# Performance work log

Measured on AMD Instinct MI355X. Metric: run time of the kernel, lower is better.

Reference implementation:

```python
import jax, jax.numpy as jnp
import numpy as np
from jax import lax

B_, DIM, H, W, Dd = 2, 256, 16, 16, 16
DI, N, DTR, K = 256, 8, 16, 4   # d_inner (expand=1), d_state, dt_rank=ceil(256/16), d_conv
OUT_C = 1200
L = H * W * Dd
EPS = 1e-5


def setup_inputs() -> dict:
    key = jax.random.key(0)
    ks = jax.random.split(key, 20)
    g = lambda k, s: jax.random.normal(k, s, jnp.float32) * 0.02
    A_log = jnp.log(jnp.broadcast_to(jnp.arange(1, N + 1, dtype=jnp.float32), (DI, N)))
    dt_bias = jnp.full((DI,), float(np.log(np.expm1(0.01))), jnp.float32)
    return {
        "input0": jax.random.normal(ks[0], (B_, DIM, H, W, Dd), jnp.float32),
        "input1": jax.random.normal(ks[1], (B_, DIM, H, W, Dd), jnp.float32),
        "norm0_w": jnp.ones((DIM,), jnp.float32),
        "norm0_b": jnp.zeros((DIM,), jnp.float32),
        "norm1_w": jnp.ones((DIM,), jnp.float32),
        "norm1_b": jnp.zeros((DIM,), jnp.float32),
        "in_proj_w": g(ks[2], (DI, DIM)),
        "in_projz_w": g(ks[3], (DI, DIM)),
        "conv1d_w": g(ks[4], (DI, 1, K)),
        "conv1d_bias": jnp.zeros((DI,), jnp.float32),
        "conv1db_w": g(ks[5], (DI, 1, K)),
        "conv1db_bias": jnp.zeros((DI,), jnp.float32),
        "xproj_w": g(ks[6], (DTR + 2 * N, DI)),
        "xprojb_w": g(ks[7], (DTR + 2 * N, DI)),
        "dtproj_w": g(ks[8], (DI, DTR)),
        "dtproj_bias": dt_bias,
        "dtprojb_w": g(ks[9], (DI, DTR)),
        "dtprojb_bias": dt_bias,
        "A_log": A_log,
        "Ab_log": A_log,
        "D_p": jnp.ones((DI,), jnp.float32),
        "D_b": jnp.ones((DI,), jnp.float32),
        "rms_w": jnp.ones((DI,), jnp.float32),
        "out_proj_w": g(ks[10], (DIM, DI)),
        "conv3d_w": g(ks[11], (OUT_C, DIM)),
        "conv3d_bias": jnp.zeros((OUT_C,), jnp.float32),
    }


def _layernorm(x, w, b):
    m = x.mean(-1, keepdims=True)
    v = ((x - m) ** 2).mean(-1, keepdims=True)
    return (x - m) * lax.rsqrt(v + EPS) * w + b


def _rmsnorm(x, w):
    return x * lax.rsqrt((x * x).mean(-1, keepdims=True) + EPS) * w


def _ssm_dir(x, z, conv_w, conv_b, xproj_w, dtproj_w, dtproj_bias, A_log, Dp):
    # One direction of the bimamba-v2 selective scan. x, z: (b, L, d_inner)
    xt = x.transpose(0, 2, 1)  # (b, d, L)
    xc = lax.conv_general_dilated(xt, conv_w, (1,), [(K - 1, 0)], feature_group_count=DI)
    x = jax.nn.silu(xc + conv_b[None, :, None]).transpose(0, 2, 1)  # causal dw-conv + silu
    dbl = x @ xproj_w.T                                   # (b, L, dt_rank + 2n)
    dt, Bm, Cm = dbl[..., :DTR], dbl[..., DTR:DTR + N], dbl[..., DTR + N:]
    dt = jax.nn.softplus(dt @ dtproj_w.T + dtproj_bias)    # (b, L, d)
    A = -jnp.exp(A_log)                                    # (d, n)
    dA = jnp.exp(dt[..., None] * A)                        # (b, L, d, n)
    dBu = (dt * x)[..., None] * Bm[:, :, None, :]          # (b, L, d, n)

    def step(h, inp):
        dA_t, dBu_t, C_t = inp
        h = h * dA_t + dBu_t
        return h, jnp.einsum('bdn,bn->bd', h, C_t)

    h0 = jnp.zeros((x.shape[0], DI, N), x.dtype)
    _, ys = lax.scan(step, h0, (dA.transpose(1, 0, 2, 3), dBu.transpose(1, 0, 2, 3), Cm.transpose(1, 0, 2)))
    y = ys.transpose(1, 0, 2) + x * Dp                     # (b, L, d)
    return y * jax.nn.silu(z)                              # gate from the matching branch


def _forward(input0, input1, norm0_w, norm0_b, norm1_w, norm1_b, in_proj_w, in_projz_w,
             conv1d_w, conv1d_bias, conv1db_w, conv1db_bias, xproj_w, xprojb_w,
             dtproj_w, dtproj_bias, dtprojb_w, dtprojb_bias, A_log, Ab_log,
             D_p, D_b, rms_w, out_proj_w, conv3d_w, conv3d_bias):
    b = input0.shape[0]
    skip = input0
    seq0 = input0.transpose(0, 2, 3, 4, 1).reshape(b, L, DIM)  # b (h w d) c
    seq1 = input1.transpose(0, 2, 3, 4, 1).reshape(b, L, DIM)
    seq0 = _layernorm(seq0, norm0_w, norm0_b)
    seq1 = _layernorm(seq1, norm1_w, norm1_b)
    x = seq0 @ in_proj_w.T    # SSM input from input0
    z = seq1 @ in_projz_w.T   # gate from extra_emb (input1)
    y_f = _ssm_dir(x, z, conv1d_w, conv1d_bias, xproj_w, dtproj_w, dtproj_bias, A_log, D_p)
    y_b = _ssm_dir(x[:, ::-1], z[:, ::-1], conv1db_w, conv1db_bias, xprojb_w,
                   dtprojb_w, dtprojb_bias, Ab_log, D_b)[:, ::-1]

    def head(y):
        o = _rmsnorm(y, rms_w) @ out_proj_w.T              # use_norm=True, then out_proj
        o = o.reshape(b, H, W, Dd, DIM).transpose(0, 4, 1, 2, 3) + skip
        return jnp.einsum('bchwd,oc->bohwd', o, conv3d_w) + conv3d_bias[None, :, None, None, None]

    out = head((y_f + y_b) * 0.5)   # if_devide_out=True
    return out, head(y_f), head(y_b)


def reference(input0, input1, norm0_w, norm0_b, norm1_w, norm1_b, in_proj_w, in_projz_w,
              conv1d_w, conv1d_bias, conv1db_w, conv1db_bias, xproj_w, xprojb_w,
              dtproj_w, dtproj_bias, dtprojb_w, dtprojb_bias, A_log, Ab_log,
              D_p, D_b, rms_w, out_proj_w, conv3d_w, conv3d_bias):
    return _forward(input0, input1, norm0_w, norm0_b, norm1_w, norm1_b, in_proj_w, in_projz_w,
                    conv1d_w, conv1d_bias, conv1db_w, conv1db_bias, xproj_w, xprojb_w,
                    dtproj_w, dtproj_bias, dtprojb_w, dtprojb_bias, A_log, Ab_log,
                    D_p, D_b, rms_w, out_proj_w, conv3d_w, conv3d_bias)
```

## Files before the change

kernel.cpp:

```cpp
#include <hip/hip_runtime.h>
#include <cstdint>

#define NTOK 8192

typedef __attribute__((ext_vector_type(4))) float f32x4;
typedef __attribute__((ext_vector_type(8))) short s16x8;
typedef __attribute__((ext_vector_type(4))) short s16x4;

__device__ __forceinline__ short f2bf(float f) {
  union { float f; unsigned u; } x; x.f = f;
  unsigned r = x.u + 0x7FFFu + ((x.u >> 16) & 1u);
  return (short)(r >> 16);
}
__device__ __forceinline__ float bf2f(short s) {
  union { float f; unsigned u; } x;
  x.u = ((unsigned)(unsigned short)s) << 16;
  return x.f;
}
__device__ __forceinline__ void gl_lds16(const void* g, void* l) {
  __builtin_amdgcn_global_load_lds((const unsigned int*)g, (unsigned int*)l, 16, 0, 0);
}

__global__ __launch_bounds__(256) void ln_transpose_kernel(
    const float* __restrict__ in0, const float* __restrict__ in1,
    const float* __restrict__ w0, const float* __restrict__ b0,
    const float* __restrict__ w1, const float* __restrict__ b1,
    const float* __restrict__ wxp, const float* __restrict__ wzp,
    const float* __restrict__ wop, const float* __restrict__ wcp,
    short* __restrict__ Wx, short* __restrict__ Wz,
    short* __restrict__ Wo, short* __restrict__ Wc,
    short* __restrict__ xlnz, float* __restrict__ seqT)
{
  __shared__ float tile[32 * 257];
  __shared__ float mu[32], rs[32];
  const int tid  = threadIdx.x;
  const int pass = blockIdx.x >> 8;
  const int b    = (blockIdx.x >> 7) & 1;
  const int l0   = (blockIdx.x & 127) << 5;

  {
    int base = (int)blockIdx.x << 10;
    #pragma unroll
    for (int i = 0; i < 4; ++i) {
      int idx = base + (i << 8) + tid;
      if (idx < 65536)       Wx[idx] = f2bf(wxp[idx]);
      else if (idx < 131072) Wz[idx - 65536] = f2bf(wzp[idx - 65536]);
      else if (idx < 196608) Wo[idx - 131072] = f2bf(wop[idx - 131072]);
      else {
        int k = idx - 196608;
        Wc[k] = ((k >> 8) < 1200) ? f2bf(wcp[k]) : (short)0;
      }
    }
  }

  const float* in = pass ? in1 : in0;
  #pragma unroll 8
  for (int i = 0; i < 32; ++i) {
    int e = (i << 8) + tid;
    int c = e >> 5, lo = e & 31;
    tile[lo * 257 + c] = in[((size_t)(b * 256 + c) << 12) + l0 + lo];
  }
  __syncthreads();
  if (tid < 64) {
    int r = tid & 31, hh = tid >> 5;
    float s = 0.f, ss = 0.f;
    #pragma unroll 16
    for (int c = hh * 128; c < hh * 128 + 128; ++c) {
      float v = tile[r * 257 + c];
      s += v; ss += v * v;
    }
    s  += __shfl_xor(s, 32, 64);
    ss += __shfl_xor(ss, 32, 64);
    if (hh == 0) {
      float m = s * (1.f / 256.f);
      mu[r] = m;
      rs[r] = rsqrtf(ss * (1.f / 256.f) - m * m + 1e-5f);
    }
  }
  __syncthreads();
  const float* w  = pass ? w1 : w0;
  const float* bb = pass ? b1 : b0;
  float wv = w[tid], bv = bb[tid];
  #pragma unroll 8
  for (int i = 0; i < 32; ++i) {
    float v = tile[i * 257 + tid];
    int row = (pass ? 8192 : 0) + (b << 12) + l0 + i;
    xlnz[(size_t)row * 256 + tid] = f2bf((v - mu[i]) * rs[i] * wv + bv);
    if (pass == 0) seqT[(((size_t)b << 12) + l0 + i) * 256 + tid] = v;
  }
}

template <int EPI>
__global__ __launch_bounds__(256) void gemm_fast(
    const short* __restrict__ A, const short* __restrict__ W0,
    const short* __restrict__ W1, float* __restrict__ Cf,
    short* __restrict__ Cb, const float* __restrict__ ADD,
    const float* __restrict__ bias, int Msplit)
{
  __shared__ short As[2][4096];
  __shared__ short Bs[2][4096];
  const int tid  = threadIdx.x;
  const int lane = tid & 63, wave = tid >> 6;
  const int m0 = blockIdx.y << 7;
  const int n0 = blockIdx.x << 7;
  const short* W = (EPI == 0 && m0 >= Msplit) ? W1 : W0;

  const int sr = tid >> 2;
  const int sc = (tid & 3) << 3;
  const int mf = lane & 15, kq = lane >> 4;
  const int wm = (wave & 1) << 6, wn = (wave >> 1) << 6;

  const short* Ar0 = A + (size_t)(m0 + sr) * 256 + sc;
  const short* Ar1 = A + (size_t)(m0 + 64 + sr) * 256 + sc;
  const short* Br0 = W + (size_t)(n0 + sr) * 256 + sc;
  const short* Br1 = W + (size_t)(n0 + 64 + sr) * 256 + sc;
  const int wo = wave << 9;

  f32x4 acc[4][4] = {};

  gl_lds16(Ar0, &As[0][wo]);
  gl_lds16(Ar1, &As[0][wo + 2048]);
  gl_lds16(Br0, &Bs[0][wo]);
  gl_lds16(Br1, &Bs[0][wo + 2048]);
  __syncthreads();

  #pragma unroll
  for (int t = 0; t < 8; ++t) {
    const int cur = t & 1;
    if (t < 7) {
      const int kt = (t + 1) << 5;
      gl_lds16(Ar0 + kt, &As[cur ^ 1][wo]);
      gl_lds16(Ar1 + kt, &As[cur ^ 1][wo + 2048]);
      gl_lds16(Br0 + kt, &Bs[cur ^ 1][wo]);
      gl_lds16(Br1 + kt, &Bs[cur ^ 1][wo + 2048]);
    }
    s16x8 af[4], bfr[4];
    #pragma unroll
    for (int i = 0; i < 4; ++i)
      af[i] = *(const s16x8*)&As[cur][((wm + (i << 4) + mf) << 5) + (kq << 3)];
    #pragma unroll
    for (int j = 0; j < 4; ++j)
      bfr[j] = *(const s16x8*)&Bs[cur][((wn + (j << 4) + mf) << 5) + (kq << 3)];
    #pragma unroll
    for (int i = 0; i < 4; ++i)
      #pragma unroll
      for (int j = 0; j < 4; ++j)
        acc[i][j] = __builtin_amdgcn_mfma_f32_16x16x32_bf16(af[i], bfr[j], acc[i][j], 0, 0, 0);
    __syncthreads();
  }

  if (EPI == 0) {
    #pragma unroll
    for (int i = 0; i < 4; ++i) {
      int gm = m0 + wm + (i << 4) + (kq << 2);
      #pragma unroll
      for (int j = 0; j < 4; ++j) {
        int gn = n0 + wn + (j << 4) + mf;
        #pragma unroll
        for (int r = 0; r < 4; ++r)
          Cf[(size_t)(gm + r) * 256 + gn] = acc[i][j][r];
      }
    }
  } else if (EPI == 1) {
    #pragma unroll
    for (int i = 0; i < 4; ++i) {
      int gm = m0 + wm + (i << 4) + (kq << 2);
      #pragma unroll
      for (int j = 0; j < 4; ++j) {
        int gn = n0 + wn + (j << 4) + mf;
        #pragma unroll
        for (int r = 0; r < 4; ++r) {
          int tok = (gm + r) & 8191;
          float v = acc[i][j][r] + ADD[(size_t)tok * 256 + gn];
          Cb[(size_t)(gm + r) * 256 + gn] = f2bf(v);
        }
      }
    }
  } else {
    const int head = m0 >> 13, bb = (m0 >> 12) & 1, lb = m0 & 4095;
    float* obase = Cf + (size_t)head * (2u * 1200u * 4096u) + (size_t)bb * (1200u * 4096u);
    #pragma unroll
    for (int i = 0; i < 4; ++i) {
      int l = lb + wm + (i << 4) + (kq << 2);
      #pragma unroll
      for (int j = 0; j < 4; ++j) {
        int gn = n0 + wn + (j << 4) + mf;
        if (gn < 1200) {
          float bv = bias[gn];
          f32x4 v = acc[i][j];
          v[0] += bv; v[1] += bv; v[2] += bv; v[3] += bv;
          __builtin_nontemporal_store(v, (f32x4*)&obase[(size_t)gn * 4096 + l]);
        }
      }
    }
  }
}

__global__ __launch_bounds__(256) void fused_front(
    const float* __restrict__ x,
    const float* __restrict__ cw0, const float* __restrict__ cb0,
    const float* __restrict__ cw1, const float* __restrict__ cb1,
    const float* __restrict__ xw0, const float* __restrict__ xw1,
    const float* __restrict__ dtw0, const float* __restrict__ dtb0,
    const float* __restrict__ dtw1, const float* __restrict__ dtb1,
    const float* __restrict__ Alog0, const float* __restrict__ Alog1,
    float* __restrict__ xcg, float* __restrict__ dblg,
    float* __restrict__ P, float* __restrict__ Q)
{
  __shared__ float xcs[16 * 256];
  __shared__ short wxs[256 * 33];
  __shared__ float dls[512];
  const int tid = threadIdx.x;
  const int dir = blockIdx.x >> 9;
  const int b   = (blockIdx.x >> 8) & 1;
  const int ch  = blockIdx.x & 255;
  const int t0  = ch << 4;
  const float* cw   = dir ? cw1 : cw0;
  const float* cb   = dir ? cb1 : cb0;
  const float* xw   = dir ? xw1 : xw0;
  const float* dtw  = dir ? dtw1 : dtw0;
  const float* dtb  = dir ? dtb1 : dtb0;
  const float* Alog = dir ? Alog1 : Alog0;
  const size_t dS = (size_t)dir * (NTOK * 256);
  const size_t xb = ((size_t)b) << 12;

  {
    const int d = tid;
    const float w0 = cw[(d << 2)], w1 = cw[(d << 2) + 1],
                w2 = cw[(d << 2) + 2], w3 = cw[(d << 2) + 3];
    const float bias = cb[d];
    float h0 = 0.f, h1 = 0.f, h2 = 0.f;
    #pragma unroll
    for (int i = 0; i < 3; ++i) {
      int ts = t0 - 3 + i; float v = 0.f;
      if (ts >= 0) { int tn = dir ? 4095 - ts : ts; v = x[(xb + tn) * 256 + d]; }
      h0 = h1; h1 = h2; h2 = v;
    }
    #pragma unroll
    for (int s = 0; s < 16; ++s) {
      int ts = t0 + s;
      int tn = dir ? 4095 - ts : ts;
      float xv = x[(xb + tn) * 256 + d];
      float a = bias + w0 * h0 + w1 * h1 + w2 * h2 + w3 * xv;
      h0 = h1; h1 = h2; h2 = xv;
      float v = a / (1.f + __expf(-a));
      xcs[s * 256 + d] = v;
      xcg[dS + (xb + ts) * 256 + d] = v;
    }
  }
  #pragma unroll
  for (int i = 0; i < 32; ++i) {
    int flat = (i << 8) + tid;
    wxs[(flat & 255) * 33 + (flat >> 8)] = f2bf(xw[flat]);
  }
  __syncthreads();

  {
    const int j = tid & 31, s0 = tid >> 5;
    float a0 = 0.f, a1 = 0.f;
    #pragma unroll 8
    for (int r = 0; r < 256; ++r) {
      float w = bf2f(wxs[r * 33 + j]);
      a0 = fmaf(xcs[s0 * 256 + r], w, a0);
      a1 = fmaf(xcs[(s0 + 8) * 256 + r], w, a1);
    }
    dls[(s0 << 5) + j] = a0;
    dls[((s0 + 8) << 5) + j] = a1;
    size_t db = (size_t)dir * 262144 + ((xb + t0) << 5);
    dblg[db + tid] = a0;
    dblg[db + 256 + tid] = a1;
  }
  __syncthreads();

  {
    const int d = tid;
    float wrow[16];
    #pragma unroll
    for (int r = 0; r < 16; ++r) wrow[r] = dtw[(d << 4) + r];
    const float bias = dtb[d];
    float Av[8], p[8], q[8];
    #pragma unroll
    for (int n = 0; n < 8; ++n) {
      Av[n] = -expf(Alog[(d << 3) + n]); p[n] = 1.f; q[n] = 0.f;
    }
    for (int s = 0; s < 16; ++s) {
      float a = bias;
      #pragma unroll
      for (int r = 0; r < 16; ++r) a = fmaf(dls[(s << 5) + r], wrow[r], a);
      float dtv = (a > 20.f) ? a : log1pf(__expf(a));
      float xv = xcs[s * 256 + d];
      float du = dtv * xv;
      #pragma unroll
      for (int n = 0; n < 8; ++n) {
        float dA = __expf(dtv * Av[n]);
        p[n] *= dA;
        q[n] = fmaf(q[n], dA, du * dls[(s << 5) + 16 + n]);
      }
    }
    size_t ob = (size_t)dir * 1048576 + ((size_t)((b << 8) + ch) * 8) * 256 + d;
    #pragma unroll
    for (int n = 0; n < 8; ++n) { P[ob + (n << 8)] = p[n]; Q[ob + (n << 8)] = q[n]; }
  }
}

__global__ __launch_bounds__(64) void scan_p2(
    const float* __restrict__ P, const float* __restrict__ Q, float* __restrict__ Hs)
{
  const int d   = ((blockIdx.x & 3) << 6) + threadIdx.x;
  const int bid = blockIdx.x >> 2;
  const int dir = bid >> 4, b = (bid >> 3) & 1, n = bid & 7;
  const size_t dOff = (size_t)dir * 1048576;
  float h = 0.f;
  #pragma unroll 8
  for (int ch = 0; ch < 256; ++ch) {
    size_t i = dOff + ((size_t)((b << 8) + ch) * 8 + n) * 256 + d;
    Hs[i] = h;
    h = fmaf(P[i], h, Q[i]);
  }
}

__global__ __launch_bounds__(256) void scan_p3(
    const float* __restrict__ xcg, const float* __restrict__ dblg,
    const float* __restrict__ dtw0, const float* __restrict__ dtb0,
    const float* __restrict__ dtw1, const float* __restrict__ dtb1,
    const float* __restrict__ Hs, const float* __restrict__ z,
    const float* __restrict__ Alog0, const float* __restrict__ Alog1,
    const float* __restrict__ Dp0, const float* __restrict__ Dp1,
    short* __restrict__ yall)
{
  __shared__ float dl[512];
  const int d = threadIdx.x;
  const int dir = blockIdx.x >> 9;
  const int b   = (blockIdx.x >> 8) & 1;
  const int ch  = blockIdx.x & 255;
  const int t0  = ch << 4;
  const float* dtw  = dir ? dtw1 : dtw0;
  const float* dtb  = dir ? dtb1 : dtb0;
  const float* Alog = dir ? Alog1 : Alog0;
  const float* Dp   = dir ? Dp1 : Dp0;
  const size_t dS = (size_t)dir * (NTOK * 256);
  const size_t xb = ((size_t)b) << 12;
  short* y = yall + (size_t)dir * (NTOK * 256);

  size_t db = (size_t)dir * 262144 + ((xb + t0) << 5);
  dl[d]       = dblg[db + d];
  dl[256 + d] = dblg[db + 256 + d];
  float wrow[16];
  #pragma unroll
  for (int r = 0; r < 16; ++r) wrow[r] = dtw[(d << 4) + r];
  const float bias = dtb[d];
  float Av[8], h[8];
  #pragma unroll
  for (int n = 0; n < 8; ++n) Av[n] = -expf(Alog[(d << 3) + n]);
  size_t hb = (size_t)dir * 1048576 + ((size_t)((b << 8) + ch) * 8) * 256 + d;
  #pragma unroll
  for (int n = 0; n < 8; ++n) h[n] = Hs[hb + (n << 8)];
  const float Dv = Dp[d];
  __syncthreads();
  for (int s = 0; s < 16; ++s) {
    float a = bias;
    #pragma unroll
    for (int r = 0; r < 16; ++r) a = fmaf(dl[(s << 5) + r], wrow[r], a);
    float dtv = (a > 20.f) ? a : log1pf(__expf(a));
    int ts = t0 + s;
    float xv = xcg[dS + (xb + ts) * 256 + d];
    float du = dtv * xv;
    float yv = 0.f;
    #pragma unroll
    for (int n = 0; n < 8; ++n) {
      float dA = __expf(dtv * Av[n]);
      h[n] = fmaf(h[n], dA, du * dl[(s << 5) + 16 + n]);
      yv = fmaf(h[n], dl[(s << 5) + 24 + n], yv);
    }
    yv = fmaf(xv, Dv, yv);
    int tn = dir ? (4095 - ts) : ts;
    size_t zi = (xb + tn) * 256 + d;
    float zv = z[zi];
    y[zi] = f2bf(yv * zv / (1.f + __expf(-zv)));
  }
}

__global__ __launch_bounds__(256) void rms_all(
    const short* __restrict__ yf, const short* __restrict__ yb,
    const float* __restrict__ w, short* __restrict__ yn)
{
  const int lane = threadIdx.x & 63, wave = threadIdx.x >> 6;
  const int mode = blockIdx.y;
  const size_t tok = ((size_t)blockIdx.x << 2) + wave;
  const size_t base = tok * 256 + (lane << 2);
  float v0, v1, v2, v3;
  if (mode == 0) {
    s16x4 a = *(const s16x4*)&yf[base];
    s16x4 c = *(const s16x4*)&yb[base];
    v0 = 0.5f * (bf2f(a[0]) + bf2f(c[0]));
    v1 = 0.5f * (bf2f(a[1]) + bf2f(c[1]));
    v2 = 0.5f * (bf2f(a[2]) + bf2f(c[2]));
    v3 = 0.5f * (bf2f(a[3]) + bf2f(c[3]));
  } else {
    const short* yy = (mode == 1) ? yf : yb;
    s16x4 a = *(const s16x4*)&yy[base];
    v0 = bf2f(a[0]); v1 = bf2f(a[1]); v2 = bf2f(a[2]); v3 = bf2f(a[3]);
  }
  float ss = v0 * v0 + v1 * v1 + v2 * v2 + v3 * v3;
  #pragma unroll
  for (int o = 32; o > 0; o >>= 1) ss += __shfl_xor(ss, o, 64);
  float sc = rsqrtf(ss * (1.f / 256.f) + 1e-5f);
  f32x4 wv = *(const f32x4*)&w[lane << 2];
  s16x4 r;
  r[0] = f2bf(v0 * sc * wv[0]);
  r[1] = f2bf(v1 * sc * wv[1]);
  r[2] = f2bf(v2 * sc * wv[2]);
  r[3] = f2bf(v3 * sc * wv[3]);
  *(s16x4*)&yn[((size_t)mode * 8192 + tok) * 256 + (lane << 2)] = r;
}

extern "C" void kernel_launch(void* const* d_in, const int* in_sizes, int n_in,
                              void* d_out, int out_size, void* d_ws, size_t ws_size,
                              hipStream_t stream) {
  const float* in0        = (const float*)d_in[0];
  const float* in1        = (const float*)d_in[1];
  const float* n0w        = (const float*)d_in[2];
  const float* n0b        = (const float*)d_in[3];
  const float* n1w        = (const float*)d_in[4];
  const float* n1b        = (const float*)d_in[5];
  const float* in_proj_w  = (const float*)d_in[6];
  const float* in_projz_w = (const float*)d_in[7];
  const float* conv1d_w   = (const float*)d_in[8];
  const float* conv1d_b   = (const float*)d_in[9];
  const float* conv1db_w  = (const float*)d_in[10];
  const float* conv1db_b  = (const float*)d_in[11];
  const float* xproj_w    = (const float*)d_in[12];
  const float* xprojb_w   = (const float*)d_in[13];
  const float* dtproj_w   = (const float*)d_in[14];
  const float* dtproj_b   = (const float*)d_in[15];
  const float* dtprojb_w  = (const float*)d_in[16];
  const float* dtprojb_b  = (const float*)d_in[17];
  const float* A_log      = (const float*)d_in[18];
  const float* Ab_log     = (const float*)d_in[19];
  const float* D_p        = (const float*)d_in[20];
  const float* D_b        = (const float*)d_in[21];
  const float* rms_w      = (const float*)d_in[22];
  const float* out_proj_w = (const float*)d_in[23];
  const float* conv3d_w   = (const float*)d_in[24];
  const float* conv3d_b   = (const float*)d_in[25];
  (void)in_sizes; (void)n_in; (void)out_size; (void)ws_size;

  float* ws = (float*)d_ws;
  size_t o = 0;
  short* xlnz = (short*)(ws + o); o += 2097152;
  float* seqT = ws + o;           o += 2097152;
  float* x    = ws + o;           o += 2097152;
  float* z    = ws + o;           o += 2097152;
  float* xc2  = ws + o;           o += 4194304;
  float* dbl2 = ws + o;           o += 524288;
  float* P    = ws + o;           o += 2097152;
  float* Q    = ws + o;           o += 2097152;
  float* Hs   = ws + o;           o += 2097152;
  short* yall = (short*)(ws + o); o += 2097152;
  short* yn   = (short*)(ws + o); o += 3145728;
  short* obuf = (short*)(ws + o); o += 3145728;
  short* Wx   = (short*)(ws + o); o += 32768;
  short* Wz   = (short*)(ws + o); o += 32768;
  short* Wo   = (short*)(ws + o); o += 32768;
  short* Wc   = (short*)(ws + o); o += 163840;
  float* out  = (float*)d_out;

  dim3 blk(256);

  ln_transpose_kernel<<<dim3(512), blk, 0, stream>>>(
      in0, in1, n0w, n0b, n1w, n1b,
      in_proj_w, in_projz_w, out_proj_w, conv3d_w, Wx, Wz, Wo, Wc,
      xlnz, seqT);

  gemm_fast<0><<<dim3(2, 128), blk, 0, stream>>>(xlnz, Wx, Wz, x, nullptr, nullptr, nullptr, 8192);

  fused_front<<<dim3(1024), blk, 0, stream>>>(
      x, conv1d_w, conv1d_b, conv1db_w, conv1db_b,
      xproj_w, xprojb_w, dtproj_w, dtproj_b, dtprojb_w, dtprojb_b,
      A_log, Ab_log, xc2, dbl2, P, Q);

  scan_p2<<<dim3(128), dim3(64), 0, stream>>>(P, Q, Hs);

  scan_p3<<<dim3(1024), blk, 0, stream>>>(
      xc2, dbl2, dtproj_w, dtproj_b, dtprojb_w, dtprojb_b,
      Hs, z, A_log, Ab_log, D_p, D_b, yall);

  rms_all<<<dim3(2048, 3), blk, 0, stream>>>(yall, yall + 2097152, rms_w, yn);
  gemm_fast<1><<<dim3(2, 192), blk, 0, stream>>>(yn, Wo, nullptr, nullptr, obuf, seqT, nullptr, 0);
  gemm_fast<2><<<dim3(10, 192), blk, 0, stream>>>(obuf, Wc, nullptr, out, nullptr, nullptr, conv3d_b, 0);
}
```

Baseline: 342.9 us.

## Fuse chunked scan phases via decoupled look-back and fold RMSNorm into out-proj GEMM

Merges the three selective-scan phases (chunk summaries, serial carry propagation, output pass) into one kernel. Blocks publish per-chunk (P,Q) and inclusive prefixes through global flags, and each block looks back over predecessors to get its incoming state. This removes the xc/dbl round trip through global memory and two launches. Separately, the RMS normalization is computed inside the out_proj GEMM's A-tile load, which drops the rms_all kernel and its yn buffer. The cost is spin-waiting that depends on blocks being scheduled in order (deadlock risk if they are not), plus the normalization being recomputed per N-tile.

```diff
diff --git a/kernel.cpp b/kernel.cpp
--- a/kernel.cpp
+++ b/kernel.cpp
@@ -29,7 +29,8 @@
     const float* __restrict__ wop, const float* __restrict__ wcp,
     short* __restrict__ Wx, short* __restrict__ Wz,
     short* __restrict__ Wo, short* __restrict__ Wc,
-    short* __restrict__ xlnz, float* __restrict__ seqT)
+    short* __restrict__ xlnz, float* __restrict__ seqT,
+    int* __restrict__ flags)
 {
   __shared__ float tile[32 * 257];
   __shared__ float mu[32], rs[32];
@@ -37,6 +38,11 @@
   const int pass = blockIdx.x >> 8;
   const int b    = (blockIdx.x >> 7) & 1;
   const int l0   = (blockIdx.x & 127) << 5;
+
+  if (blockIdx.x == 0) {
+    #pragma unroll
+    for (int i = 0; i < 4; ++i) flags[(i << 8) + tid] = 0;
+  }
 
   {
     int base = (int)blockIdx.x << 10;
@@ -196,7 +202,7 @@
   }
 }
 
-__global__ __launch_bounds__(256) void fused_front(
+__global__ __launch_bounds__(256, 4) void fused_scan(
     const float* __restrict__ x,
     const float* __restrict__ cw0, const float* __restrict__ cb0,
     const float* __restrict__ cw1, const float* __restrict__ cb1,
@@ -204,16 +210,21 @@
     const float* __restrict__ dtw0, const float* __restrict__ dtb0,
     const float* __restrict__ dtw1, const float* __restrict__ dtb1,
     const float* __restrict__ Alog0, const float* __restrict__ Alog1,
-    float* __restrict__ xcg, float* __restrict__ dblg,
-    float* __restrict__ P, float* __restrict__ Q)
+    const float* __restrict__ Dp0, const float* __restrict__ Dp1,
+    const float* __restrict__ z,
+    float* __restrict__ P, float* __restrict__ Q, float* __restrict__ Pref,
+    int* __restrict__ flags, short* __restrict__ yall)
 {
   __shared__ float xcs[16 * 256];
   __shared__ short wxs[256 * 33];
   __shared__ float dls[512];
+  __shared__ int stat;
   const int tid = threadIdx.x;
   const int dir = blockIdx.x >> 9;
   const int b   = (blockIdx.x >> 8) & 1;
   const int ch  = blockIdx.x & 255;
+  const int gb  = (dir << 1) | b;
+  const int fi  = (gb << 8) + ch;
   const int t0  = ch << 4;
   const float* cw   = dir ? cw1 : cw0;
   const float* cb   = dir ? cb1 : cb0;
@@ -221,8 +232,9 @@
   const float* dtw  = dir ? dtw1 : dtw0;
   const float* dtb  = dir ? dtb1 : dtb0;
   const float* Alog = dir ? Alog1 : Alog0;
-  const size_t dS = (size_t)dir * (NTOK * 256);
+  const float* Dp   = dir ? Dp1 : Dp0;
   const size_t xb = ((size_t)b) << 12;
+  short* yout = yall + (size_t)dir * (NTOK * 256);
 
   {
     const int d = tid;
@@ -243,9 +255,7 @@
       float xv = x[(xb + tn) * 256 + d];
       float a = bias + w0 * h0 + w1 * h1 + w2 * h2 + w3 * xv;
       h0 = h1; h1 = h2; h2 = xv;
-      float v = a / (1.f + __expf(-a));
-      xcs[s * 256 + d] = v;
-      xcg[dS + (xb + ts) * 256 + d] = v;
+      xcs[s * 256 + d] = a / (1.f + __expf(-a));
     }
   }
   #pragma unroll
@@ -266,152 +276,231 @@
     }
     dls[(s0 << 5) + j] = a0;
     dls[((s0 + 8) << 5) + j] = a1;
-    size_t db = (size_t)dir * 262144 + ((xb + t0) << 5);
-    dblg[db + tid] = a0;
-    dblg[db + 256 + tid] = a1;
-  }
-  __syncthreads();
-
-  {
-    const int d = tid;
-    float wrow[16];
-    #pragma unroll
-    for (int r = 0; r < 16; ++r) wrow[r] = dtw[(d << 4) + r];
-    const float bias = dtb[d];
-    float Av[8], p[8], q[8];
-    #pragma unroll
-    for (int n = 0; n < 8; ++n) {
-      Av[n] = -expf(Alog[(d << 3) + n]); p[n] = 1.f; q[n] = 0.f;
-    }
-    for (int s = 0; s < 16; ++s) {
-      float a = bias;
-      #pragma unroll
-      for (int r = 0; r < 16; ++r) a = fmaf(dls[(s << 5) + r], wrow[r], a);
-      float dtv = (a > 20.f) ? a : log1pf(__expf(a));
-      float xv = xcs[s * 256 + d];
-      float du = dtv * xv;
-      #pragma unroll
-      for (int n = 0; n < 8; ++n) {
-        float dA = __expf(dtv * Av[n]);
-        p[n] *= dA;
-        q[n] = fmaf(q[n], dA, du * dls[(s << 5) + 16 + n]);
-      }
-    }
-    size_t ob = (size_t)dir * 1048576 + ((size_t)((b << 8) + ch) * 8) * 256 + d;
-    #pragma unroll
-    for (int n = 0; n < 8; ++n) { P[ob + (n << 8)] = p[n]; Q[ob + (n << 8)] = q[n]; }
-  }
-}
-
-__global__ __launch_bounds__(64) void scan_p2(
-    const float* __restrict__ P, const float* __restrict__ Q, float* __restrict__ Hs)
-{
-  const int d   = ((blockIdx.x & 3) << 6) + threadIdx.x;
-  const int bid = blockIdx.x >> 2;
-  const int dir = bid >> 4, b = (bid >> 3) & 1, n = bid & 7;
-  const size_t dOff = (size_t)dir * 1048576;
-  float h = 0.f;
-  #pragma unroll 8
-  for (int ch = 0; ch < 256; ++ch) {
-    size_t i = dOff + ((size_t)((b << 8) + ch) * 8 + n) * 256 + d;
-    Hs[i] = h;
-    h = fmaf(P[i], h, Q[i]);
-  }
-}
-
-__global__ __launch_bounds__(256) void scan_p3(
-    const float* __restrict__ xcg, const float* __restrict__ dblg,
-    const float* __restrict__ dtw0, const float* __restrict__ dtb0,
-    const float* __restrict__ dtw1, const float* __restrict__ dtb1,
-    const float* __restrict__ Hs, const float* __restrict__ z,
-    const float* __restrict__ Alog0, const float* __restrict__ Alog1,
-    const float* __restrict__ Dp0, const float* __restrict__ Dp1,
-    short* __restrict__ yall)
-{
-  __shared__ float dl[512];
-  const int d = threadIdx.x;
-  const int dir = blockIdx.x >> 9;
-  const int b   = (blockIdx.x >> 8) & 1;
-  const int ch  = blockIdx.x & 255;
-  const int t0  = ch << 4;
-  const float* dtw  = dir ? dtw1 : dtw0;
-  const float* dtb  = dir ? dtb1 : dtb0;
-  const float* Alog = dir ? Alog1 : Alog0;
-  const float* Dp   = dir ? Dp1 : Dp0;
-  const size_t dS = (size_t)dir * (NTOK * 256);
-  const size_t xb = ((size_t)b) << 12;
-  short* y = yall + (size_t)dir * (NTOK * 256);
-
-  size_t db = (size_t)dir * 262144 + ((xb + t0) << 5);
-  dl[d]       = dblg[db + d];
-  dl[256 + d] = dblg[db + 256 + d];
+  }
+  __syncthreads();
+
+  const int d = tid;
   float wrow[16];
   #pragma unroll
   for (int r = 0; r < 16; ++r) wrow[r] = dtw[(d << 4) + r];
   const float bias = dtb[d];
-  float Av[8], h[8];
-  #pragma unroll
-  for (int n = 0; n < 8; ++n) Av[n] = -expf(Alog[(d << 3) + n]);
-  size_t hb = (size_t)dir * 1048576 + ((size_t)((b << 8) + ch) * 8) * 256 + d;
-  #pragma unroll
-  for (int n = 0; n < 8; ++n) h[n] = Hs[hb + (n << 8)];
   const float Dv = Dp[d];
-  __syncthreads();
+  float Av[8], p[8], q[8];
+  #pragma unroll
+  for (int n = 0; n < 8; ++n) {
+    Av[n] = -expf(Alog[(d << 3) + n]); p[n] = 1.f; q[n] = 0.f;
+  }
   for (int s = 0; s < 16; ++s) {
     float a = bias;
     #pragma unroll
-    for (int r = 0; r < 16; ++r) a = fmaf(dl[(s << 5) + r], wrow[r], a);
+    for (int r = 0; r < 16; ++r) a = fmaf(dls[(s << 5) + r], wrow[r], a);
+    float dtv = (a > 20.f) ? a : log1pf(__expf(a));
+    float xv = xcs[s * 256 + d];
+    float du = dtv * xv;
+    #pragma unroll
+    for (int n = 0; n < 8; ++n) {
+      float dA = __expf(dtv * Av[n]);
+      p[n] *= dA;
+      q[n] = fmaf(q[n], dA, du * dls[(s << 5) + 16 + n]);
+    }
+  }
+
+  const size_t ab = ((size_t)fi << 11) + d;
+  #pragma unroll
+  for (int n = 0; n < 8; ++n) { P[ab + (n << 8)] = p[n]; Q[ab + (n << 8)] = q[n]; }
+  __syncthreads();
+
+  float hin[8];
+  if (ch == 0) {
+    #pragma unroll
+    for (int n = 0; n < 8; ++n) { hin[n] = 0.f; Pref[ab + (n << 8)] = q[n]; }
+  } else {
+    if (tid == 0)
+      __hip_atomic_store(&flags[fi], 1, __ATOMIC_RELEASE, __HIP_MEMORY_SCOPE_AGENT);
+    float Pa[8], Qa[8];
+    #pragma unroll
+    for (int n = 0; n < 8; ++n) { Pa[n] = 1.f; Qa[n] = 0.f; }
+    int j = ch - 1;
+    for (;;) {
+      __syncthreads();
+      if (tid == 0) {
+        int f;
+        for (;;) {
+          f = __hip_atomic_load(&flags[(gb << 8) + j], __ATOMIC_RELAXED,
+                                __HIP_MEMORY_SCOPE_AGENT);
+          if (f >= 1) break;
+          __builtin_amdgcn_s_sleep(2);
+        }
+        f = __hip_atomic_load(&flags[(gb << 8) + j], __ATOMIC_ACQUIRE,
+                              __HIP_MEMORY_SCOPE_AGENT);
+        stat = f;
+      }
+      __syncthreads();
+      const int st = stat;
+      const size_t jb = (((size_t)((gb << 8) + j)) << 11) + d;
+      if (st == 2) {
+        #pragma unroll
+        for (int n = 0; n < 8; ++n)
+          hin[n] = fmaf(Pa[n], Pref[jb + (n << 8)], Qa[n]);
+        break;
+      }
+      #pragma unroll
+      for (int n = 0; n < 8; ++n) {
+        float Pj = P[jb + (n << 8)], Qj = Q[jb + (n << 8)];
+        Qa[n] = fmaf(Pa[n], Qj, Qa[n]);
+        Pa[n] *= Pj;
+      }
+      --j;
+    }
+    #pragma unroll
+    for (int n = 0; n < 8; ++n) Pref[ab + (n << 8)] = fmaf(p[n], hin[n], q[n]);
+  }
+  __syncthreads();
+  if (tid == 0)
+    __hip_atomic_store(&flags[fi], 2, __ATOMIC_RELEASE, __HIP_MEMORY_SCOPE_AGENT);
+
+  float h[8];
+  #pragma unroll
+  for (int n = 0; n < 8; ++n) h[n] = hin[n];
+  for (int s = 0; s < 16; ++s) {
+    float a = bias;
+    #pragma unroll
+    for (int r = 0; r < 16; ++r) a = fmaf(dls[(s << 5) + r], wrow[r], a);
     float dtv = (a > 20.f) ? a : log1pf(__expf(a));
     int ts = t0 + s;
-    float xv = xcg[dS + (xb + ts) * 256 + d];
+    float xv = xcs[s * 256 + d];
     float du = dtv * xv;
     float yv = 0.f;
     #pragma unroll
     for (int n = 0; n < 8; ++n) {
       float dA = __expf(dtv * Av[n]);
-      h[n] = fmaf(h[n], dA, du * dl[(s << 5) + 16 + n]);
-      yv = fmaf(h[n], dl[(s << 5) + 24 + n], yv);
+      h[n] = fmaf(h[n], dA, du * dls[(s << 5) + 16 + n]);
+      yv = fmaf(h[n], dls[(s << 5) + 24 + n], yv);
     }
     yv = fmaf(xv, Dv, yv);
     int tn = dir ? (4095 - ts) : ts;
     size_t zi = (xb + tn) * 256 + d;
     float zv = z[zi];
-    y[zi] = f2bf(yv * zv / (1.f + __expf(-zv)));
-  }
-}
-
-__global__ __launch_bounds__(256) void rms_all(
-    const short* __restrict__ yf, const short* __restrict__ yb,
-    const float* __restrict__ w, short* __restrict__ yn)
+    yout[zi] = f2bf(yv * zv / (1.f + __expf(-zv)));
+  }
+}
+
+__global__ __launch_bounds__(256) void gemm_rms_epi1(
+    const short* __restrict__ yall, const short* __restrict__ W0,
+    const float* __restrict__ rmsw, short* __restrict__ Cb,
+    const float* __restrict__ ADD)
 {
-  const int lane = threadIdx.x & 63, wave = threadIdx.x >> 6;
-  const int mode = blockIdx.y;
-  const size_t tok = ((size_t)blockIdx.x << 2) + wave;
-  const size_t base = tok * 256 + (lane << 2);
-  float v0, v1, v2, v3;
-  if (mode == 0) {
-    s16x4 a = *(const s16x4*)&yf[base];
-    s16x4 c = *(const s16x4*)&yb[base];
-    v0 = 0.5f * (bf2f(a[0]) + bf2f(c[0]));
-    v1 = 0.5f * (bf2f(a[1]) + bf2f(c[1]));
-    v2 = 0.5f * (bf2f(a[2]) + bf2f(c[2]));
-    v3 = 0.5f * (bf2f(a[3]) + bf2f(c[3]));
-  } else {
-    const short* yy = (mode == 1) ? yf : yb;
-    s16x4 a = *(const s16x4*)&yy[base];
-    v0 = bf2f(a[0]); v1 = bf2f(a[1]); v2 = bf2f(a[2]); v3 = bf2f(a[3]);
-  }
-  float ss = v0 * v0 + v1 * v1 + v2 * v2 + v3 * v3;
-  #pragma unroll
-  for (int o = 32; o > 0; o >>= 1) ss += __shfl_xor(ss, o, 64);
-  float sc = rsqrtf(ss * (1.f / 256.f) + 1e-5f);
-  f32x4 wv = *(const f32x4*)&w[lane << 2];
-  s16x4 r;
-  r[0] = f2bf(v0 * sc * wv[0]);
-  r[1] = f2bf(v1 * sc * wv[1]);
-  r[2] = f2bf(v2 * sc * wv[2]);
-  r[3] = f2bf(v3 * sc * wv[3]);
-  *(s16x4*)&yn[((size_t)mode * 8192 + tok) * 256 + (lane << 2)] = r;
+  __shared__ short As[4096];
+  __shared__ short Bs[4096];
+  __shared__ float scale[128];
+  __shared__ float rw[256];
+  const int tid  = threadIdx.x;
+  const int lane = tid & 63, wave = tid >> 6;
+  const int m0 = blockIdx.y << 7;
+  const int n0 = blockIdx.x << 7;
+  const int mode = m0 >> 13;
+  const int tok0 = m0 & 8191;
+  const short* yf = yall;
+  const short* yb = yall + 2097152;
+  const short* ysel = (mode == 1) ? yf : yb;
+
+  rw[tid] = rmsw[tid];
+
+  for (int rr = 0; rr < 32; ++rr) {
+    int r = (rr << 2) + wave;
+    size_t base = (size_t)(tok0 + r) * 256 + (lane << 2);
+    float v0, v1, v2, v3;
+    if (mode == 0) {
+      s16x4 a = *(const s16x4*)&yf[base];
+      s16x4 c = *(const s16x4*)&yb[base];
+      v0 = 0.5f * (bf2f(a[0]) + bf2f(c[0]));
+      v1 = 0.5f * (bf2f(a[1]) + bf2f(c[1]));
+      v2 = 0.5f * (bf2f(a[2]) + bf2f(c[2]));
+      v3 = 0.5f * (bf2f(a[3]) + bf2f(c[3]));
+    } else {
+      s16x4 a = *(const s16x4*)&ysel[base];
+      v0 = bf2f(a[0]); v1 = bf2f(a[1]); v2 = bf2f(a[2]); v3 = bf2f(a[3]);
+    }
+    float ss = v0 * v0 + v1 * v1 + v2 * v2 + v3 * v3;
+    #pragma unroll
+    for (int o = 32; o > 0; o >>= 1) ss += __shfl_xor(ss, o, 64);
+    if (lane == 0) scale[r] = rsqrtf(ss * (1.f / 256.f) + 1e-5f);
+  }
+  __syncthreads();
+
+  const int sr = tid >> 2;
+  const int sc = (tid & 3) << 3;
+  const int mf = lane & 15, kq = lane >> 4;
+  const int wm = (wave & 1) << 6, wn = (wave >> 1) << 6;
+  const short* Br0 = W0 + (size_t)(n0 + sr) * 256 + sc;
+  const short* Br1 = W0 + (size_t)(n0 + 64 + sr) * 256 + sc;
+  const int wo = wave << 9;
+
+  const int ar = tid >> 1;
+  const int ac = (tid & 1) << 4;
+  const size_t abase = (size_t)(tok0 + ar) * 256 + ac;
+  const float s_r = scale[ar];
+
+  f32x4 acc[4][4] = {};
+
+  for (int t = 0; t < 8; ++t) {
+    const int kt = t << 5;
+    {
+      s16x8 o0, o1;
+      if (mode == 0) {
+        s16x8 f0 = *(const s16x8*)&yf[abase + kt];
+        s16x8 f1 = *(const s16x8*)&yf[abase + kt + 8];
+        s16x8 c0 = *(const s16x8*)&yb[abase + kt];
+        s16x8 c1 = *(const s16x8*)&yb[abase + kt + 8];
+        #pragma unroll
+        for (int e = 0; e < 8; ++e) {
+          o0[e] = f2bf((0.5f * (bf2f(f0[e]) + bf2f(c0[e])) * s_r) * rw[kt + ac + e]);
+          o1[e] = f2bf((0.5f * (bf2f(f1[e]) + bf2f(c1[e])) * s_r) * rw[kt + ac + 8 + e]);
+        }
+      } else {
+        s16x8 f0 = *(const s16x8*)&ysel[abase + kt];
+        s16x8 f1 = *(const s16x8*)&ysel[abase + kt + 8];
+        #pragma unroll
+        for (int e = 0; e < 8; ++e) {
+          o0[e] = f2bf((bf2f(f0[e]) * s_r) * rw[kt + ac + e]);
+          o1[e] = f2bf((bf2f(f1[e]) * s_r) * rw[kt + ac + 8 + e]);
+        }
+      }
+      *(s16x8*)&As[(ar << 5) + ac]     = o0;
+      *(s16x8*)&As[(ar << 5) + ac + 8] = o1;
+    }
+    gl_lds16(Br0 + kt, &Bs[wo]);
+    gl_lds16(Br1 + kt, &Bs[wo + 2048]);
+    __syncthreads();
+    s16x8 af[4], bfr[4];
+    #pragma unroll
+    for (int i = 0; i < 4; ++i)
+      af[i] = *(const s16x8*)&As[((wm + (i << 4) + mf) << 5) + (kq << 3)];
+    #pragma unroll
+    for (int j = 0; j < 4; ++j)
+      bfr[j] = *(const s16x8*)&Bs[((wn + (j << 4) + mf) << 5) + (kq << 3)];
+    #pragma unroll
+    for (int i = 0; i < 4; ++i)
+      #pragma unroll
+      for (int j = 0; j < 4; ++j)
+        acc[i][j] = __builtin_amdgcn_mfma_f32_16x16x32_bf16(af[i], bfr[j], acc[i][j], 0, 0, 0);
+    __syncthreads();
+  }
+
+  #pragma unroll
+  for (int i = 0; i < 4; ++i) {
+    int gm = m0 + wm + (i << 4) + (kq << 2);
+    #pragma unroll
+    for (int j = 0; j < 4; ++j) {
+      int gn = n0 + wn + (j << 4) + mf;
+      #pragma unroll
+      for (int r = 0; r < 4; ++r) {
+        int tok = (gm + r) & 8191;
+        float v = acc[i][j][r] + ADD[(size_t)tok * 256 + gn];
+        Cb[(size_t)(gm + r) * 256 + gn] = f2bf(v);
+      }
+    }
+  }
 }
 
 extern "C" void kernel_launch(void* const* d_in, const int* in_sizes, int n_in,
@@ -451,18 +540,16 @@
   float* seqT = ws + o;           o += 2097152;
   float* x    = ws + o;           o += 2097152;
   float* z    = ws + o;           o += 2097152;
-  float* xc2  = ws + o;           o += 4194304;
-  float* dbl2 = ws + o;           o += 524288;
   float* P    = ws + o;           o += 2097152;
   float* Q    = ws + o;           o += 2097152;
-  float* Hs   = ws + o;           o += 2097152;
+  float* Pref = ws + o;           o += 2097152;
   short* yall = (short*)(ws + o); o += 2097152;
-  short* yn   = (short*)(ws + o); o += 3145728;
   short* obuf = (short*)(ws + o); o += 3145728;
   short* Wx   = (short*)(ws + o); o += 32768;
   short* Wz   = (short*)(ws + o); o += 32768;
   short* Wo   = (short*)(ws + o); o += 32768;
   short* Wc   = (short*)(ws + o); o += 163840;
+  int*   flags = (int*)(ws + o);  o += 1024;
   float* out  = (float*)d_out;
 
   dim3 blk(256);
@@ -470,22 +557,15 @@
   ln_transpose_kernel<<<dim3(512), blk, 0, stream>>>(
       in0, in1, n0w, n0b, n1w, n1b,
       in_proj_w, in_projz_w, out_proj_w, conv3d_w, Wx, Wz, Wo, Wc,
-      xlnz, seqT);
+      xlnz, seqT, flags);
 
   gemm_fast<0><<<dim3(2, 128), blk, 0, stream>>>(xlnz, Wx, Wz, x, nullptr, nullptr, nullptr, 8192);
 
-  fused_front<<<dim3(1024), blk, 0, stream>>>(
+  fused_scan<<<dim3(1024), blk, 0, stream>>>(
       x, conv1d_w, conv1d_b, conv1db_w, conv1db_b,
       xproj_w, xprojb_w, dtproj_w, dtproj_b, dtprojb_w, dtprojb_b,
-      A_log, Ab_log, xc2, dbl2, P, Q);
-
-  scan_p2<<<dim3(128), dim3(64), 0, stream>>>(P, Q, Hs);
-
-  scan_p3<<<dim3(1024), blk, 0, stream>>>(
-      xc2, dbl2, dtproj_w, dtproj_b, dtprojb_w, dtprojb_b,
-      Hs, z, A_log, Ab_log, D_p, D_b, yall);
-
-  rms_all<<<dim3(2048, 3), blk, 0, stream>>>(yall, yall + 2097152, rms_w, yn);
-  gemm_fast<1><<<dim3(2, 192), blk, 0, stream>>>(yn, Wo, nullptr, nullptr, obuf, seqT, nullptr, 0);
+      A_log, Ab_log, D_p, D_b, z, P, Q, Pref, flags, yall);
+
+  gemm_rms_epi1<<<dim3(2, 192), blk, 0, stream>>>(yall, Wo, rms_w, obuf, seqT);
   gemm_fast<2><<<dim3(10, 192), blk, 0, stream>>>(obuf, Wc, nullptr, out, nullptr, nullptr, conv3d_b, 0);
 }
```

Measured after the change: 504.4 us. +47.1%, slower.

## Fuse RMSNorm into out_proj GEMM and read skip directly from input

Applied to the files above, without the earlier changes.

Removes the standalone rms_all kernel and the yn buffer by computing per-row RMS scales inside the out_proj GEMM and normalizing A tiles while staging them into LDS. Also stops writing the transposed seqT skip copy in the layernorm kernel; the GEMM epilogue now reads the skip directly from input0 in channel-major layout. This saves a kernel launch and several large buffer round-trips. In exchange, each GEMM block recomputes row norms, and each A tile is rebuilt twice because n has two tiles. The A stage is also single-buffered with synchronous loads.

```diff
diff --git a/kernel.cpp b/kernel.cpp
--- a/kernel.cpp
+++ b/kernel.cpp
@@ -29,7 +29,7 @@
     const float* __restrict__ wop, const float* __restrict__ wcp,
     short* __restrict__ Wx, short* __restrict__ Wz,
     short* __restrict__ Wo, short* __restrict__ Wc,
-    short* __restrict__ xlnz, float* __restrict__ seqT)
+    short* __restrict__ xlnz)
 {
   __shared__ float tile[32 * 257];
   __shared__ float mu[32], rs[32];
@@ -86,7 +86,6 @@
     float v = tile[i * 257 + tid];
     int row = (pass ? 8192 : 0) + (b << 12) + l0 + i;
     xlnz[(size_t)row * 256 + tid] = f2bf((v - mu[i]) * rs[i] * wv + bv);
-    if (pass == 0) seqT[(((size_t)b << 12) + l0 + i) * 256 + tid] = v;
   }
 }
 
@@ -159,21 +158,6 @@
         #pragma unroll
         for (int r = 0; r < 4; ++r)
           Cf[(size_t)(gm + r) * 256 + gn] = acc[i][j][r];
-      }
-    }
-  } else if (EPI == 1) {
-    #pragma unroll
-    for (int i = 0; i < 4; ++i) {
-      int gm = m0 + wm + (i << 4) + (kq << 2);
-      #pragma unroll
-      for (int j = 0; j < 4; ++j) {
-        int gn = n0 + wn + (j << 4) + mf;
-        #pragma unroll
-        for (int r = 0; r < 4; ++r) {
-          int tok = (gm + r) & 8191;
-          float v = acc[i][j][r] + ADD[(size_t)tok * 256 + gn];
-          Cb[(size_t)(gm + r) * 256 + gn] = f2bf(v);
-        }
       }
     }
   } else {
@@ -380,38 +364,124 @@
   }
 }
 
-__global__ __launch_bounds__(256) void rms_all(
-    const short* __restrict__ yf, const short* __restrict__ yb,
-    const float* __restrict__ w, short* __restrict__ yn)
+__global__ __launch_bounds__(256) void gemm_rms_epi1(
+    const short* __restrict__ yall, const short* __restrict__ W0,
+    const float* __restrict__ rmsw, short* __restrict__ Cb,
+    const float* __restrict__ in0)
 {
-  const int lane = threadIdx.x & 63, wave = threadIdx.x >> 6;
-  const int mode = blockIdx.y;
-  const size_t tok = ((size_t)blockIdx.x << 2) + wave;
-  const size_t base = tok * 256 + (lane << 2);
-  float v0, v1, v2, v3;
-  if (mode == 0) {
-    s16x4 a = *(const s16x4*)&yf[base];
-    s16x4 c = *(const s16x4*)&yb[base];
-    v0 = 0.5f * (bf2f(a[0]) + bf2f(c[0]));
-    v1 = 0.5f * (bf2f(a[1]) + bf2f(c[1]));
-    v2 = 0.5f * (bf2f(a[2]) + bf2f(c[2]));
-    v3 = 0.5f * (bf2f(a[3]) + bf2f(c[3]));
-  } else {
-    const short* yy = (mode == 1) ? yf : yb;
-    s16x4 a = *(const s16x4*)&yy[base];
-    v0 = bf2f(a[0]); v1 = bf2f(a[1]); v2 = bf2f(a[2]); v3 = bf2f(a[3]);
-  }
-  float ss = v0 * v0 + v1 * v1 + v2 * v2 + v3 * v3;
+  __shared__ short As[4096];
+  __shared__ short Bs[4096];
+  __shared__ float scale[128];
+  __shared__ float rw[256];
+  const int tid  = threadIdx.x;
+  const int lane = tid & 63, wave = tid >> 6;
+  const int m0 = blockIdx.y << 7;
+  const int n0 = blockIdx.x << 7;
+  const int mode = m0 >> 13;
+  const int tok0 = m0 & 8191;
+  const short* yf = yall;
+  const short* yb = yall + 2097152;
+  const short* ysel = (mode == 1) ? yf : yb;
+
+  rw[tid] = rmsw[tid];
+
+  for (int rr = 0; rr < 32; ++rr) {
+    int r = (rr << 2) + wave;
+    size_t base = (size_t)(tok0 + r) * 256 + (lane << 2);
+    float v0, v1, v2, v3;
+    if (mode == 0) {
+      s16x4 a = *(const s16x4*)&yf[base];
+      s16x4 c = *(const s16x4*)&yb[base];
+      v0 = 0.5f * (bf2f(a[0]) + bf2f(c[0]));
+      v1 = 0.5f * (bf2f(a[1]) + bf2f(c[1]));
+      v2 = 0.5f * (bf2f(a[2]) + bf2f(c[2]));
+      v3 = 0.5f * (bf2f(a[3]) + bf2f(c[3]));
+    } else {
+      s16x4 a = *(const s16x4*)&ysel[base];
+      v0 = bf2f(a[0]); v1 = bf2f(a[1]); v2 = bf2f(a[2]); v3 = bf2f(a[3]);
+    }
+    float ss = v0 * v0 + v1 * v1 + v2 * v2 + v3 * v3;
+    #pragma unroll
+    for (int o = 32; o > 0; o >>= 1) ss += __shfl_xor(ss, o, 64);
+    if (lane == 0) scale[r] = rsqrtf(ss * (1.f / 256.f) + 1e-5f);
+  }
+  __syncthreads();
+
+  const int sr = tid >> 2;
+  const int sc = (tid & 3) << 3;
+  const int mf = lane & 15, kq = lane >> 4;
+  const int wm = (wave & 1) << 6, wn = (wave >> 1) << 6;
+  const short* Br0 = W0 + (size_t)(n0 + sr) * 256 + sc;
+  const short* Br1 = W0 + (size_t)(n0 + 64 + sr) * 256 + sc;
+  const int wo = wave << 9;
+
+  const int ar = tid >> 1;
+  const int ac = (tid & 1) << 4;
+  const size_t abase = (size_t)(tok0 + ar) * 256 + ac;
+  const float s_r = scale[ar];
+
+  f32x4 acc[4][4] = {};
+
+  for (int t = 0; t < 8; ++t) {
+    const int kt = t << 5;
+    {
+      s16x8 o0, o1;
+      if (mode == 0) {
+        s16x8 f0 = *(const s16x8*)&yf[abase + kt];
+        s16x8 f1 = *(const s16x8*)&yf[abase + kt + 8];
+        s16x8 c0 = *(const s16x8*)&yb[abase + kt];
+        s16x8 c1 = *(const s16x8*)&yb[abase + kt + 8];
+        #pragma unroll
+        for (int e = 0; e < 8; ++e) {
+          o0[e] = f2bf((0.5f * (bf2f(f0[e]) + bf2f(c0[e])) * s_r) * rw[kt + ac + e]);
+          o1[e] = f2bf((0.5f * (bf2f(f1[e]) + bf2f(c1[e])) * s_r) * rw[kt + ac + 8 + e]);
+        }
+      } else {
+        s16x8 f0 = *(const s16x8*)&ysel[abase + kt];
+        s16x8 f1 = *(const s16x8*)&ysel[abase + kt + 8];
+        #pragma unroll
+        for (int e = 0; e < 8; ++e) {
+          o0[e] = f2bf((bf2f(f0[e]) * s_r) * rw[kt + ac + e]);
+          o1[e] = f2bf((bf2f(f1[e]) * s_r) * rw[kt + ac + 8 + e]);
+        }
+      }
+      *(s16x8*)&As[(ar << 5) + ac]     = o0;
+      *(s16x8*)&As[(ar << 5) + ac + 8] = o1;
+    }
+    gl_lds16(Br0 + kt, &Bs[wo]);
+    gl_lds16(Br1 + kt, &Bs[wo + 2048]);
+    __syncthreads();
+    s16x8 af[4], bfr[4];
+    #pragma unroll
+    for (int i = 0; i < 4; ++i)
+      af[i] = *(const s16x8*)&As[((wm + (i << 4) + mf) << 5) + (kq << 3)];
+    #pragma unroll
+    for (int j = 0; j < 4; ++j)
+      bfr[j] = *(const s16x8*)&Bs[((wn + (j << 4) + mf) << 5) + (kq << 3)];
+    #pragma unroll
+    for (int i = 0; i < 4; ++i)
+      #pragma unroll
+      for (int j = 0; j < 4; ++j)
+        acc[i][j] = __builtin_amdgcn_mfma_f32_16x16x32_bf16(af[i], bfr[j], acc[i][j], 0, 0, 0);
+    __syncthreads();
+  }
+
   #pragma unroll
-  for (int o = 32; o > 0; o >>= 1) ss += __shfl_xor(ss, o, 64);
-  float sc = rsqrtf(ss * (1.f / 256.f) + 1e-5f);
-  f32x4 wv = *(const f32x4*)&w[lane << 2];
-  s16x4 r;
-  r[0] = f2bf(v0 * sc * wv[0]);
-  r[1] = f2bf(v1 * sc * wv[1]);
-  r[2] = f2bf(v2 * sc * wv[2]);
-  r[3] = f2bf(v3 * sc * wv[3]);
-  *(s16x4*)&yn[((size_t)mode * 8192 + tok) * 256 + (lane << 2)] = r;
+  for (int i = 0; i < 4; ++i) {
+    int gm = m0 + wm + (i << 4) + (kq << 2);
+    int tok = gm & 8191;
+    int bb2 = tok >> 12, ll = tok & 4095;
+    #pragma unroll
+    for (int j = 0; j < 4; ++j) {
+      int gn = n0 + wn + (j << 4) + mf;
+      f32x4 sk = *(const f32x4*)&in0[((((size_t)(bb2 << 8)) + gn) << 12) + ll];
+      #pragma unroll
+      for (int r = 0; r < 4; ++r) {
+        float v = acc[i][j][r] + sk[r];
+        Cb[(size_t)(gm + r) * 256 + gn] = f2bf(v);
+      }
+    }
+  }
 }
 
 extern "C" void kernel_launch(void* const* d_in, const int* in_sizes, int n_in,
@@ -448,7 +518,6 @@
   float* ws = (float*)d_ws;
   size_t o = 0;
   short* xlnz = (short*)(ws + o); o += 2097152;
-  float* seqT = ws + o;           o += 2097152;
   float* x    = ws + o;           o += 2097152;
   float* z    = ws + o;           o += 2097152;
   float* xc2  = ws + o;           o += 4194304;
@@ -457,7 +526,6 @@
   float* Q    = ws + o;           o += 2097152;
   float* Hs   = ws + o;           o += 2097152;
   short* yall = (short*)(ws + o); o += 2097152;
-  short* yn   = (short*)(ws + o); o += 3145728;
   short* obuf = (short*)(ws + o); o += 3145728;
   short* Wx   = (short*)(ws + o); o += 32768;
   short* Wz   = (short*)(ws + o); o += 32768;
@@ -470,7 +538,7 @@
   ln_transpose_kernel<<<dim3(512), blk, 0, stream>>>(
       in0, in1, n0w, n0b, n1w, n1b,
       in_proj_w, in_projz_w, out_proj_w, conv3d_w, Wx, Wz, Wo, Wc,
-      xlnz, seqT);
+      xlnz);
 
   gemm_fast<0><<<dim3(2, 128), blk, 0, stream>>>(xlnz, Wx, Wz, x, nullptr, nullptr, nullptr, 8192);
 
@@ -485,7 +553,6 @@
       xc2, dbl2, dtproj_w, dtproj_b, dtprojb_w, dtprojb_b,
       Hs, z, A_log, Ab_log, D_p, D_b, yall);
 
-  rms_all<<<dim3(2048, 3), blk, 0, stream>>>(yall, yall + 2097152, rms_w, yn);
-  gemm_fast<1><<<dim3(2, 192), blk, 0, stream>>>(yn, Wo, nullptr, nullptr, obuf, seqT, nullptr, 0);
+  gemm_rms_epi1<<<dim3(2, 192), blk, 0, stream>>>(yall, Wo, rms_w, obuf, in0);
   gemm_fast<2><<<dim3(10, 192), blk, 0, stream>>>(obuf, Wc, nullptr, out, nullptr, nullptr, conv3d_b, 0);
 }
```

Result: no change. 345.5 us (+0.8%).
